# Kernel optimization log

Hardware: AMD Instinct MI355X
Metric: run time of the kernel (lower is better)

## Reference

```python
import jax, jax.numpy as jnp
import numpy as np

EPS = 1e-6  # flax.linen.LayerNorm default

def layer_norm(x, scale, bias):
    mean = jnp.mean(x, axis=-1, keepdims=True)
    var = jnp.mean(jnp.square(x - mean), axis=-1, keepdims=True)
    return (x - mean) * jax.lax.rsqrt(var + EPS) * scale + bias

def setup_inputs() -> dict:
    key = jax.random.key(0)
    ks = jax.random.split(key, 4)
    B, P, D, H = 2, 2048, 768, 12
    hd = D // H
    x = jax.random.normal(ks[0], (B, P, D), dtype=jnp.float32)
    W_qkv = jax.random.normal(ks[1], (D, 3 * D), dtype=jnp.float32) * (D ** -0.5)
    W_out = jax.random.normal(ks[2], (D, D), dtype=jnp.float32) * (D ** -0.5)
    b_out = jnp.zeros((D,), dtype=jnp.float32)
    return {
        "x": x,
        "W_qkv": W_qkv,
        "q_scale": jnp.ones((hd,), jnp.float32),
        "q_bias": jnp.zeros((hd,), jnp.float32),
        "k_scale": jnp.ones((hd,), jnp.float32),
        "k_bias": jnp.zeros((hd,), jnp.float32),
        "o_scale": jnp.ones((D,), jnp.float32),
        "o_bias": jnp.zeros((D,), jnp.float32),
        "W_out": W_out,
        "b_out": b_out,
    }

def reference(x, W_qkv, q_scale, q_bias, k_scale, k_bias, o_scale, o_bias, W_out, b_out):
    B, P, D = x.shape
    H = 12
    hd = D // H
    scale = hd ** -0.5
    # fused QKV projection, no bias
    qkv = (x @ W_qkv).reshape(B, P, 3, H, hd).transpose(2, 0, 3, 1, 4)  # [3,B,H,P,hd]
    q, k, v = qkv[0], qkv[1], qkv[2]
    # per-head QK LayerNorm over head_dim
    q = layer_norm(q, q_scale, q_bias) * scale
    k = layer_norm(k, k_scale, k_bias)
    attn = jnp.einsum("bhqd,bhkd->bhqk", q, k)
    attn = jax.nn.softmax(attn, axis=-1)
    out = jnp.einsum("bhqk,bhkd->bhqd", attn, v)  # [B,H,P,hd]
    out = jnp.swapaxes(out, 1, 2).reshape(B, P, D)
    out = layer_norm(out, o_scale, o_bias)
    return out @ W_out + b_out
```

## Files before the change

kernel.cpp:

```cpp
#include <hip/hip_runtime.h>
#include <hip/hip_bf16.h>

#define B_  2
#define P_  2048
#define D_  768
#define H_  12
#define HD_ 64
#define M_  (B_ * P_)
#define N1_ (3 * D_)

typedef __attribute__((ext_vector_type(8))) short short8;
typedef __attribute__((ext_vector_type(4))) float f32x4;
typedef __attribute__((ext_vector_type(16))) float f32x16;
typedef __attribute__((ext_vector_type(4))) unsigned u32x4;
typedef unsigned short ushort;

__device__ __forceinline__ ushort f2bf(float f) {
    unsigned u = __float_as_uint(f);
    u += 0x7fffu + ((u >> 16) & 1u);
    return (ushort)(u >> 16);
}

__device__ __forceinline__ unsigned cvtpk(float a, float b) {
    unsigned r;
    asm("v_cvt_pk_bf16_f32 %0, %1, %2" : "=v"(r) : "v"(a), "v"(b));
    return r;
}

__device__ __forceinline__ float bf2f(ushort u) {
    return __uint_as_float((unsigned)u << 16);
}

__device__ __forceinline__ int swap23(int s) {
    return (s & ~12) | ((s & 4) << 1) | ((s & 8) >> 1);
}

#define QSC_ (0.125f * 1.44269504088896340736f)

__global__ __launch_bounds__(512) void gemm_qkv_mfma(
        const float* __restrict__ x, const float* __restrict__ w,
        const float* __restrict__ qs, const float* __restrict__ qb,
        const float* __restrict__ ks, const float* __restrict__ kb,
        ushort* __restrict__ qkv) {
    __shared__ __align__(16) ushort As[128][40];
    __shared__ __align__(16) ushort Bs[128][40];

    const int tid  = threadIdx.x;
    const int lane = tid & 63;
    const int wv   = tid >> 6;
    const int quad = lane >> 4;
    const int col  = lane & 15;
    const int wr   = (wv >> 1) * 32;
    const int wc   = (wv & 1) * 64;
    const int rowBase = blockIdx.y * 128;
    const int colBase = blockIdx.x * 128;

    const int am0 = tid >> 3, ac4 = tid & 7;
    const int nB  = tid & 127, kq = tid >> 7;

    float4 apre[2];
    float  bpre[8];
    auto load_tile = [&](int kt) {
        const int k0 = kt * 32;
        apre[0] = *(const float4*)(x + (size_t)(rowBase + am0) * D_ + k0 + ac4 * 4);
        apre[1] = *(const float4*)(x + (size_t)(rowBase + am0 + 64) * D_ + k0 + ac4 * 4);
#pragma unroll
        for (int j = 0; j < 8; j++)
            bpre[j] = w[(size_t)(k0 + kq * 8 + j) * N1_ + colBase + nB];
    };

    f32x4 acc[2][4];
#pragma unroll
    for (int i = 0; i < 2; i++)
#pragma unroll
        for (int j = 0; j < 4; j++) acc[i][j] = (f32x4){0.f, 0.f, 0.f, 0.f};

    load_tile(0);
    const int NT = D_ / 32;
    for (int kt = 0; kt < NT; kt++) {
        __syncthreads();
        {
            uint2 a0 = {cvtpk(apre[0].x, apre[0].y), cvtpk(apre[0].z, apre[0].w)};
            uint2 a1 = {cvtpk(apre[1].x, apre[1].y), cvtpk(apre[1].z, apre[1].w)};
            *(uint2*)&As[am0][ac4 * 4]      = a0;
            *(uint2*)&As[am0 + 64][ac4 * 4] = a1;
            u32x4 bb;
#pragma unroll
            for (int j = 0; j < 4; j++) bb[j] = cvtpk(bpre[2 * j], bpre[2 * j + 1]);
            *(u32x4*)&Bs[nB][kq * 8] = bb;
        }
        __syncthreads();
        if (kt + 1 < NT) load_tile(kt + 1);

        short8 af[2], bf[4];
#pragma unroll
        for (int mt = 0; mt < 2; mt++) af[mt] = *(const short8*)&As[wr + mt * 16 + col][quad * 8];
#pragma unroll
        for (int nt = 0; nt < 4; nt++) bf[nt] = *(const short8*)&Bs[wc + nt * 16 + col][quad * 8];
#pragma unroll
        for (int mt = 0; mt < 2; mt++)
#pragma unroll
            for (int nt = 0; nt < 4; nt++)
                acc[mt][nt] = __builtin_amdgcn_mfma_f32_16x16x32_bf16(af[mt], bf[nt], acc[mt][nt], 0, 0, 0);
    }

    const int comp = colBase / D_;
    const int rem  = colBase + wc - comp * D_;
    const int h    = rem >> 6;
    float sc4[4] = {0, 0, 0, 0}, bi4[4] = {0, 0, 0, 0};
    if (comp == 0) {
#pragma unroll
        for (int nt = 0; nt < 4; nt++) { sc4[nt] = qs[nt * 16 + col]; bi4[nt] = qb[nt * 16 + col]; }
    } else if (comp == 1) {
#pragma unroll
        for (int nt = 0; nt < 4; nt++) { sc4[nt] = ks[nt * 16 + col]; bi4[nt] = kb[nt * 16 + col]; }
    }

#pragma unroll
    for (int mt = 0; mt < 2; mt++) {
#pragma unroll
        for (int r = 0; r < 4; r++) {
            int m  = rowBase + wr + mt * 16 + quad * 4 + r;
            int bb = m >> 11;
            int p  = m & 2047;
            float v0 = acc[mt][0][r], v1 = acc[mt][1][r], v2 = acc[mt][2][r], v3 = acc[mt][3][r];
            if (comp < 2) {
                float s = v0 + v1 + v2 + v3;
#pragma unroll
                for (int off = 1; off < 16; off <<= 1) s += __shfl_xor(s, off, 64);
                float mean = s * (1.0f / 64.0f);
                float d0 = v0 - mean, d1 = v1 - mean, d2 = v2 - mean, d3 = v3 - mean;
                float sq = d0 * d0 + d1 * d1 + d2 * d2 + d3 * d3;
#pragma unroll
                for (int off = 1; off < 16; off <<= 1) sq += __shfl_xor(sq, off, 64);
                float inv = rsqrtf(sq * (1.0f / 64.0f) + 1e-6f);
                v0 = d0 * inv * sc4[0] + bi4[0];
                v1 = d1 * inv * sc4[1] + bi4[1];
                v2 = d2 * inv * sc4[2] + bi4[2];
                v3 = d3 * inv * sc4[3] + bi4[3];
                if (comp == 0) { v0 *= QSC_; v1 *= QSC_; v2 *= QSC_; v3 *= QSC_; }
            }
            size_t base = ((((size_t)comp * B_ + bb) * H_ + h) * P_ + p) * HD_;
            qkv[base +  0 + col] = f2bf(v0);
            qkv[base + 16 + col] = f2bf(v1);
            qkv[base + 32 + col] = f2bf(v2);
            qkv[base + 48 + col] = f2bf(v3);
        }
    }
}

__global__ __launch_bounds__(256) void attn_split(const ushort* __restrict__ qkv,
                                                  ushort* __restrict__ o0, ushort* __restrict__ o1,
                                                  ushort* __restrict__ o2, ushort* __restrict__ o3,
                                                  float* __restrict__ l0, float* __restrict__ l1,
                                                  float* __restrict__ l2, float* __restrict__ l3) {
    const int p0  = blockIdx.x * 256;
    const int bh  = blockIdx.y;
    const int s   = blockIdx.z;
    const int nsp = gridDim.z;
    const int b   = bh / H_, h = bh % H_;
    ushort* opart = (s == 0) ? o0 : (s == 1) ? o1 : (s == 2) ? o2 : o3;
    float*  lpart = (s == 0) ? l0 : (s == 1) ? l1 : (s == 2) ? l2 : l3;
    const int tid  = threadIdx.x;
    const int lane = tid & 63;
    const int wv   = tid >> 6;
    const int half = lane >> 5;
    const int n32  = lane & 31;

    __shared__ __align__(16) ushort KVs[2][2][64][72];

    const size_t hs  = (size_t)P_ * HD_;
    const int    kv0 = s * (P_ / nsp);
    const ushort* qg = qkv + ((size_t)(0 * B_ + b) * H_ + h) * hs + (size_t)(p0 + wv * 64) * HD_;
    const ushort* kg = qkv + ((size_t)(1 * B_ + b) * H_ + h) * hs + (size_t)kv0 * HD_;
    const ushort* vg = qkv + ((size_t)(2 * B_ + b) * H_ + h) * hs + (size_t)kv0 * HD_;

    short8 aq[2][4];
#pragma unroll
    for (int qs2 = 0; qs2 < 2; qs2++)
#pragma unroll
        for (int ks2 = 0; ks2 < 4; ks2++)
            aq[qs2][ks2] = *(const short8*)(qg + (size_t)(qs2 * 32 + n32) * HD_ + ks2 * 16 + half * 8);

    float lsum[2] = {0.f, 0.f};
    f32x16 oaccT[2][2];
#pragma unroll
    for (int q2 = 0; q2 < 2; q2++)
#pragma unroll
        for (int nt = 0; nt < 2; nt++)
#pragma unroll
            for (int r = 0; r < 16; r++) oaccT[q2][nt][r] = 0.f;

    const int kr = tid >> 3, kc8 = tid & 7;
    const int krs = swap23(kr);
    const int vd = tid & 63,  vkh = tid >> 6;

    uint4  kpre[2];
    ushort vpre[16];
    auto load_tile = [&](int kt) {
        const ushort* kg_t = kg + (size_t)kt * 64 * HD_;
        const ushort* vg_t = vg + (size_t)kt * 64 * HD_;
        kpre[0] = *(const uint4*)(kg_t + (size_t)kr * HD_ + kc8 * 8);
        kpre[1] = *(const uint4*)(kg_t + (size_t)(kr + 32) * HD_ + kc8 * 8);
#pragma unroll
        for (int j = 0; j < 16; j++)
            vpre[j] = vg_t[(size_t)(vkh * 16 + j) * HD_ + vd];
    };
    auto stage = [&](int buf) {
        *(uint4*)&KVs[buf][0][krs][kc8 * 8]      = kpre[0];
        *(uint4*)&KVs[buf][0][krs + 32][kc8 * 8] = kpre[1];
        *(short8*)&KVs[buf][1][vd][vkh * 16]     = *(short8*)&vpre[0];
        *(short8*)&KVs[buf][1][vd][vkh * 16 + 8] = *(short8*)&vpre[8];
    };

    load_tile(0);
    stage(0);
    __syncthreads();

    const int NT = (P_ / 64) / nsp;
    int cur = 0;
    for (int kt = 0; kt < NT; kt++) {
        const bool more = (kt + 1 < NT);
        if (more) load_tile(kt + 1);

        ushort (*Ks)[72] = KVs[cur][0];
        ushort (*Vs)[72] = KVs[cur][1];

#pragma unroll
        for (int nt = 0; nt < 2; nt++) {
#pragma unroll
            for (int q2 = 0; q2 < 2; q2++) {
                f32x16 sc;
#pragma unroll
                for (int r = 0; r < 16; r++) sc[r] = 0.f;
                __builtin_amdgcn_s_setprio(1);
#pragma unroll
                for (int ks2 = 0; ks2 < 4; ks2++) {
                    short8 kb2 = *(const short8*)&Ks[nt * 32 + n32][ks2 * 16 + half * 8];
                    sc = __builtin_amdgcn_mfma_f32_32x32x16_bf16(kb2, aq[q2][ks2], sc, 0, 0, 0);
                }
                __builtin_amdgcn_s_setprio(0);
                float p[16];
#pragma unroll
                for (int r = 0; r < 16; r++) {
                    p[r] = __builtin_amdgcn_exp2f(sc[r]);
                    lsum[q2] += p[r];
                }
                unsigned w[8];
#pragma unroll
                for (int i = 0; i < 8; i++) w[i] = cvtpk(p[2 * i], p[2 * i + 1]);
                __builtin_amdgcn_s_setprio(1);
#pragma unroll
                for (int kp2 = 0; kp2 < 2; kp2++) {
                    u32x4 t = {w[kp2 * 4 + 0], w[kp2 * 4 + 1], w[kp2 * 4 + 2], w[kp2 * 4 + 3]};
                    short8 pb = __builtin_bit_cast(short8, t);
                    const int kstep = nt * 2 + kp2;
#pragma unroll
                    for (int ntd = 0; ntd < 2; ntd++) {
                        short8 av = *(const short8*)&Vs[ntd * 32 + n32][kstep * 16 + half * 8];
                        oaccT[q2][ntd] = __builtin_amdgcn_mfma_f32_32x32x16_bf16(av, pb, oaccT[q2][ntd], 0, 0, 0);
                    }
                }
                __builtin_amdgcn_s_setprio(0);
            }
        }

        if (more) {
            stage(cur ^ 1);
            __syncthreads();
            cur ^= 1;
        }
    }

#pragma unroll
    for (int q2 = 0; q2 < 2; q2++)
        lsum[q2] += __shfl_xor(lsum[q2], 32, 64);
    if (lane < 32) {
        lpart[(size_t)bh * P_ + p0 + wv * 64 +  0 + lane] = lsum[0];
        lpart[(size_t)bh * P_ + p0 + wv * 64 + 32 + lane] = lsum[1];
    }

    float* scr = (float*)&KVs[0][0][0][0] + wv * 1152;
#pragma unroll
    for (int q2 = 0; q2 < 2; q2++) {
#pragma unroll
        for (int ntd = 0; ntd < 2; ntd++) {
#pragma unroll
            for (int r = 0; r < 16; r++)
                scr[n32 * 36 + (r & 3) + 8 * (r >> 2) + 4 * half] = oaccT[q2][ntd][r];
#pragma unroll
            for (int i = 0; i < 4; i++) {
                int ql = i * 8 + (lane >> 3);
                int c4 = lane & 7;
                float4 v = *(const float4*)&scr[ql * 36 + c4 * 4];
                uint2 pk = {cvtpk(v.x, v.y), cvtpk(v.z, v.w)};
                *(uint2*)(opart + ((size_t)bh * P_ + p0 + wv * 64 + q2 * 32 + ql) * HD_ + ntd * 32 + c4 * 4) = pk;
            }
        }
    }
}

__global__ __launch_bounds__(256) void ln_o(const ushort* __restrict__ o0,
                                            const ushort* __restrict__ o1,
                                            const ushort* __restrict__ o2,
                                            const ushort* __restrict__ o3,
                                            const float* __restrict__ l0,
                                            const float* __restrict__ l1,
                                            const float* __restrict__ l2,
                                            const float* __restrict__ l3,
                                            const int ns,
                                            ushort* __restrict__ lnb,
                                            const float* __restrict__ osc,
                                            const float* __restrict__ ob) {
    __shared__ float red[4];
    __shared__ float red2[4];
    const int row = blockIdx.x;
    const int b   = row >> 11;
    const int p   = row & (P_ - 1);
    const int tid = threadIdx.x;

    auto src = [&](int d) {
        int h = d >> 6;
        size_t lr  = (size_t)(b * H_ + h) * P_ + p;
        size_t idx = lr * HD_ + (d & 63);
        float num = bf2f(o0[idx]) + bf2f(o1[idx]);
        float den = l0[lr] + l1[lr];
        if (ns == 4) { num += bf2f(o2[idx]) + bf2f(o3[idx]); den += l2[lr] + l3[lr]; }
        return num / den;
    };
    float v0 = src(tid);
    float v1 = src(tid + 256);
    float v2 = src(tid + 512);
    float s = v0 + v1 + v2;
#pragma unroll
    for (int o = 32; o > 0; o >>= 1) s += __shfl_xor(s, o, 64);
    if ((tid & 63) == 0) red[tid >> 6] = s;
    __syncthreads();
    float mean = (red[0] + red[1] + red[2] + red[3]) * (1.0f / 768.0f);
    float d0 = v0 - mean, d1 = v1 - mean, d2 = v2 - mean;
    float sq = d0 * d0 + d1 * d1 + d2 * d2;
#pragma unroll
    for (int o = 32; o > 0; o >>= 1) sq += __shfl_xor(sq, o, 64);
    if ((tid & 63) == 0) red2[tid >> 6] = sq;
    __syncthreads();
    float var = (red2[0] + red2[1] + red2[2] + red2[3]) * (1.0f / 768.0f);
    float inv = rsqrtf(var + 1e-6f);
    const size_t base = (size_t)row * D_;
    lnb[base + tid]       = f2bf(d0 * inv * osc[tid]       + ob[tid]);
    lnb[base + tid + 256] = f2bf(d1 * inv * osc[tid + 256] + ob[tid + 256]);
    lnb[base + tid + 512] = f2bf(d2 * inv * osc[tid + 512] + ob[tid + 512]);
}

__global__ __launch_bounds__(256) void gemm_out_mfma(
        const ushort* __restrict__ a, const float* __restrict__ w,
        const float* __restrict__ bias, float* __restrict__ out) {
    __shared__ __align__(16) ushort As[64][40];
    __shared__ __align__(16) ushort Bs[64][40];

    const int tid  = threadIdx.x;
    const int lane = tid & 63;
    const int wv   = tid >> 6;
    const int quad = lane >> 4;
    const int col  = lane & 15;
    const int wr   = (wv >> 1) * 32;
    const int wc   = (wv & 1) * 32;
    const int rowBase = blockIdx.y * 64;
    const int colBase = blockIdx.x * 64;

    const int am  = tid >> 2, ac8 = tid & 3;
    const int nB  = tid & 63, kq = tid >> 6;

    uint4 apre;
    float bpre[8];
    auto load_tile = [&](int kt) {
        const int k0 = kt * 32;
        apre = *(const uint4*)(a + (size_t)(rowBase + am) * D_ + k0 + ac8 * 8);
#pragma unroll
        for (int j = 0; j < 8; j++)
            bpre[j] = w[(size_t)(k0 + kq * 8 + j) * D_ + colBase + nB];
    };

    f32x4 acc[2][2];
#pragma unroll
    for (int i = 0; i < 2; i++)
#pragma unroll
        for (int j = 0; j < 2; j++) acc[i][j] = (f32x4){0.f, 0.f, 0.f, 0.f};

    load_tile(0);
    const int NT = D_ / 32;
    for (int kt = 0; kt < NT; kt++) {
        __syncthreads();
        *(uint4*)&As[am][ac8 * 8] = apre;
        {
            u32x4 bb;
#pragma unroll
            for (int j = 0; j < 4; j++) bb[j] = cvtpk(bpre[2 * j], bpre[2 * j + 1]);
            *(u32x4*)&Bs[nB][kq * 8] = bb;
        }
        __syncthreads();
        if (kt + 1 < NT) load_tile(kt + 1);

        short8 af[2], bf[2];
#pragma unroll
        for (int mt = 0; mt < 2; mt++) af[mt] = *(const short8*)&As[wr + mt * 16 + col][quad * 8];
#pragma unroll
        for (int nt = 0; nt < 2; nt++) bf[nt] = *(const short8*)&Bs[wc + nt * 16 + col][quad * 8];
#pragma unroll
        for (int mt = 0; mt < 2; mt++)
#pragma unroll
            for (int nt = 0; nt < 2; nt++)
                acc[mt][nt] = __builtin_amdgcn_mfma_f32_16x16x32_bf16(af[mt], bf[nt], acc[mt][nt], 0, 0, 0);
    }

    float b2[2];
#pragma unroll
    for (int nt = 0; nt < 2; nt++) b2[nt] = bias[colBase + wc + nt * 16 + col];
#pragma unroll
    for (int mt = 0; mt < 2; mt++) {
#pragma unroll
        for (int r = 0; r < 4; r++) {
            int m = rowBase + wr + mt * 16 + quad * 4 + r;
            float* dst = out + (size_t)m * D_ + colBase + wc;
#pragma unroll
            for (int nt = 0; nt < 2; nt++)
                dst[nt * 16 + col] = acc[mt][nt][r] + b2[nt];
        }
    }
}

extern "C" void kernel_launch(void* const* d_in, const int* in_sizes, int n_in,
                              void* d_out, int out_size, void* d_ws, size_t ws_size,
                              hipStream_t stream) {
    const float* x    = (const float*)d_in[0];
    const float* Wqkv = (const float*)d_in[1];
    const float* qs   = (const float*)d_in[2];
    const float* qb   = (const float*)d_in[3];
    const float* ks   = (const float*)d_in[4];
    const float* kb   = (const float*)d_in[5];
    const float* osc  = (const float*)d_in[6];
    const float* ob   = (const float*)d_in[7];
    const float* Wout = (const float*)d_in[8];
    const float* bout = (const float*)d_in[9];
    float* out = (float*)d_out;

    ushort* qkv = (ushort*)d_ws;
    const size_t qkvE = (size_t)3 * B_ * H_ * P_ * HD_;
    const size_t oE   = (size_t)B_ * H_ * P_ * HD_;
    const size_t lE   = (size_t)B_ * H_ * P_;
    ushort* obase = qkv + qkvE;
    const size_t need4 = (qkvE + 3 * oE) * sizeof(ushort) + 4 * lE * sizeof(float);
    const int nsp = (ws_size >= need4) ? 4 : 2;
    ushort* op[4];
    float* lbase;
    if (nsp == 4) {
        op[0] = obase; op[1] = obase + oE; op[2] = obase + 2 * oE; op[3] = (ushort*)out;
        lbase = (float*)(obase + 3 * oE);
    } else {
        op[0] = obase; op[1] = (ushort*)out; op[2] = obase; op[3] = obase;
        lbase = (float*)(obase + oE);
    }
    float* lp[4] = {lbase, lbase + lE, lbase + 2 * lE, lbase + 3 * lE};
    ushort* ln_buf = qkv;

    gemm_qkv_mfma<<<dim3(N1_ / 128, M_ / 128), 512, 0, stream>>>(x, Wqkv, qs, qb, ks, kb, qkv);
    attn_split<<<dim3(P_ / 256, B_ * H_, nsp), 256, 0, stream>>>(
        qkv, op[0], op[1], op[2], op[3], lp[0], lp[1], lp[2], lp[3]);
    ln_o<<<dim3(M_), 256, 0, stream>>>(
        op[0], op[1], op[2], op[3], lp[0], lp[1], lp[2], lp[3], nsp, ln_buf, osc, ob);
    gemm_out_mfma<<<dim3(D_ / 64, M_ / 64), 256, 0, stream>>>(ln_buf, Wout, bout, out);
}
```

Measured before the change: 197.4 us.

## Split attention work across eight waves of 32 queries each

The attention kernel now launches 512 threads per block, so each of eight waves owns 32 query rows instead of four waves owning 64. This halves per-thread accumulators, Q fragments and K/V prefetch registers, and each thread stages half as much of every K/V tile. The aim is more resident waves to hide LDS and global-memory latency. The cost is that each K/V fragment read from LDS now feeds half as many MFMAs, so LDS traffic per MFMA doubles. A barrier is added before the shared tile buffer is reused as output scratch.

```diff
diff --git a/kernel.cpp b/kernel.cpp
--- a/kernel.cpp
+++ b/kernel.cpp
@@ -149,7 +149,7 @@
     }
 }
 
-__global__ __launch_bounds__(256) void attn_split(const ushort* __restrict__ qkv,
+__global__ __launch_bounds__(512) void attn_split(const ushort* __restrict__ qkv,
                                                   ushort* __restrict__ o0, ushort* __restrict__ o1,
                                                   ushort* __restrict__ o2, ushort* __restrict__ o3,
                                                   float* __restrict__ l0, float* __restrict__ l1,
@@ -171,46 +171,39 @@
 
     const size_t hs  = (size_t)P_ * HD_;
     const int    kv0 = s * (P_ / nsp);
-    const ushort* qg = qkv + ((size_t)(0 * B_ + b) * H_ + h) * hs + (size_t)(p0 + wv * 64) * HD_;
+    const ushort* qg = qkv + ((size_t)(0 * B_ + b) * H_ + h) * hs + (size_t)(p0 + wv * 32) * HD_;
     const ushort* kg = qkv + ((size_t)(1 * B_ + b) * H_ + h) * hs + (size_t)kv0 * HD_;
     const ushort* vg = qkv + ((size_t)(2 * B_ + b) * H_ + h) * hs + (size_t)kv0 * HD_;
 
-    short8 aq[2][4];
-#pragma unroll
-    for (int qs2 = 0; qs2 < 2; qs2++)
-#pragma unroll
-        for (int ks2 = 0; ks2 < 4; ks2++)
-            aq[qs2][ks2] = *(const short8*)(qg + (size_t)(qs2 * 32 + n32) * HD_ + ks2 * 16 + half * 8);
-
-    float lsum[2] = {0.f, 0.f};
-    f32x16 oaccT[2][2];
-#pragma unroll
-    for (int q2 = 0; q2 < 2; q2++)
-#pragma unroll
-        for (int nt = 0; nt < 2; nt++)
-#pragma unroll
-            for (int r = 0; r < 16; r++) oaccT[q2][nt][r] = 0.f;
+    short8 aq[4];
+#pragma unroll
+    for (int ks2 = 0; ks2 < 4; ks2++)
+        aq[ks2] = *(const short8*)(qg + (size_t)n32 * HD_ + ks2 * 16 + half * 8);
+
+    float lsum = 0.f;
+    f32x16 oaccT[2];
+#pragma unroll
+    for (int nt = 0; nt < 2; nt++)
+#pragma unroll
+        for (int r = 0; r < 16; r++) oaccT[nt][r] = 0.f;
 
     const int kr = tid >> 3, kc8 = tid & 7;
     const int krs = swap23(kr);
     const int vd = tid & 63,  vkh = tid >> 6;
 
-    uint4  kpre[2];
-    ushort vpre[16];
+    uint4  kpre;
+    ushort vpre[8];
     auto load_tile = [&](int kt) {
         const ushort* kg_t = kg + (size_t)kt * 64 * HD_;
         const ushort* vg_t = vg + (size_t)kt * 64 * HD_;
-        kpre[0] = *(const uint4*)(kg_t + (size_t)kr * HD_ + kc8 * 8);
-        kpre[1] = *(const uint4*)(kg_t + (size_t)(kr + 32) * HD_ + kc8 * 8);
-#pragma unroll
-        for (int j = 0; j < 16; j++)
-            vpre[j] = vg_t[(size_t)(vkh * 16 + j) * HD_ + vd];
+        kpre = *(const uint4*)(kg_t + (size_t)kr * HD_ + kc8 * 8);
+#pragma unroll
+        for (int j = 0; j < 8; j++)
+            vpre[j] = vg_t[(size_t)(vkh * 8 + j) * HD_ + vd];
     };
     auto stage = [&](int buf) {
-        *(uint4*)&KVs[buf][0][krs][kc8 * 8]      = kpre[0];
-        *(uint4*)&KVs[buf][0][krs + 32][kc8 * 8] = kpre[1];
-        *(short8*)&KVs[buf][1][vd][vkh * 16]     = *(short8*)&vpre[0];
-        *(short8*)&KVs[buf][1][vd][vkh * 16 + 8] = *(short8*)&vpre[8];
+        *(uint4*)&KVs[buf][0][krs][kc8 * 8] = kpre;
+        *(short8*)&KVs[buf][1][vd][vkh * 8] = *(short8*)&vpre[0];
     };
 
     load_tile(0);
@@ -228,41 +221,38 @@
 
 #pragma unroll
         for (int nt = 0; nt < 2; nt++) {
-#pragma unroll
-            for (int q2 = 0; q2 < 2; q2++) {
-                f32x16 sc;
-#pragma unroll
-                for (int r = 0; r < 16; r++) sc[r] = 0.f;
-                __builtin_amdgcn_s_setprio(1);
-#pragma unroll
-                for (int ks2 = 0; ks2 < 4; ks2++) {
-                    short8 kb2 = *(const short8*)&Ks[nt * 32 + n32][ks2 * 16 + half * 8];
-                    sc = __builtin_amdgcn_mfma_f32_32x32x16_bf16(kb2, aq[q2][ks2], sc, 0, 0, 0);
+            f32x16 sc;
+#pragma unroll
+            for (int r = 0; r < 16; r++) sc[r] = 0.f;
+            __builtin_amdgcn_s_setprio(1);
+#pragma unroll
+            for (int ks2 = 0; ks2 < 4; ks2++) {
+                short8 kb2 = *(const short8*)&Ks[nt * 32 + n32][ks2 * 16 + half * 8];
+                sc = __builtin_amdgcn_mfma_f32_32x32x16_bf16(kb2, aq[ks2], sc, 0, 0, 0);
+            }
+            __builtin_amdgcn_s_setprio(0);
+            float p[16];
+#pragma unroll
+            for (int r = 0; r < 16; r++) {
+                p[r] = __builtin_amdgcn_exp2f(sc[r]);
+                lsum += p[r];
+            }
+            unsigned w[8];
+#pragma unroll
+            for (int i = 0; i < 8; i++) w[i] = cvtpk(p[2 * i], p[2 * i + 1]);
+            __builtin_amdgcn_s_setprio(1);
+#pragma unroll
+            for (int kp2 = 0; kp2 < 2; kp2++) {
+                u32x4 t = {w[kp2 * 4 + 0], w[kp2 * 4 + 1], w[kp2 * 4 + 2], w[kp2 * 4 + 3]};
+                short8 pb = __builtin_bit_cast(short8, t);
+                const int kstep = nt * 2 + kp2;
+#pragma unroll
+                for (int ntd = 0; ntd < 2; ntd++) {
+                    short8 av = *(const short8*)&Vs[ntd * 32 + n32][kstep * 16 + half * 8];
+                    oaccT[ntd] = __builtin_amdgcn_mfma_f32_32x32x16_bf16(av, pb, oaccT[ntd], 0, 0, 0);
                 }
-                __builtin_amdgcn_s_setprio(0);
-                float p[16];
-#pragma unroll
-                for (int r = 0; r < 16; r++) {
-                    p[r] = __builtin_amdgcn_exp2f(sc[r]);
-                    lsum[q2] += p[r];
-                }
-                unsigned w[8];
-#pragma unroll
-                for (int i = 0; i < 8; i++) w[i] = cvtpk(p[2 * i], p[2 * i + 1]);
-                __builtin_amdgcn_s_setprio(1);
-#pragma unroll
-                for (int kp2 = 0; kp2 < 2; kp2++) {
-                    u32x4 t = {w[kp2 * 4 + 0], w[kp2 * 4 + 1], w[kp2 * 4 + 2], w[kp2 * 4 + 3]};
-                    short8 pb = __builtin_bit_cast(short8, t);
-                    const int kstep = nt * 2 + kp2;
-#pragma unroll
-                    for (int ntd = 0; ntd < 2; ntd++) {
-                        short8 av = *(const short8*)&Vs[ntd * 32 + n32][kstep * 16 + half * 8];
-                        oaccT[q2][ntd] = __builtin_amdgcn_mfma_f32_32x32x16_bf16(av, pb, oaccT[q2][ntd], 0, 0, 0);
-                    }
-                }
-                __builtin_amdgcn_s_setprio(0);
             }
+            __builtin_amdgcn_s_setprio(0);
         }
 
         if (more) {
@@ -272,30 +262,24 @@
         }
     }
 
-#pragma unroll
-    for (int q2 = 0; q2 < 2; q2++)
-        lsum[q2] += __shfl_xor(lsum[q2], 32, 64);
-    if (lane < 32) {
-        lpart[(size_t)bh * P_ + p0 + wv * 64 +  0 + lane] = lsum[0];
-        lpart[(size_t)bh * P_ + p0 + wv * 64 + 32 + lane] = lsum[1];
-    }
-
+    lsum += __shfl_xor(lsum, 32, 64);
+    if (lane < 32)
+        lpart[(size_t)bh * P_ + p0 + wv * 32 + lane] = lsum;
+
+    __syncthreads();
     float* scr = (float*)&KVs[0][0][0][0] + wv * 1152;
 #pragma unroll
-    for (int q2 = 0; q2 < 2; q2++) {
-#pragma unroll
-        for (int ntd = 0; ntd < 2; ntd++) {
-#pragma unroll
-            for (int r = 0; r < 16; r++)
-                scr[n32 * 36 + (r & 3) + 8 * (r >> 2) + 4 * half] = oaccT[q2][ntd][r];
-#pragma unroll
-            for (int i = 0; i < 4; i++) {
-                int ql = i * 8 + (lane >> 3);
-                int c4 = lane & 7;
-                float4 v = *(const float4*)&scr[ql * 36 + c4 * 4];
-                uint2 pk = {cvtpk(v.x, v.y), cvtpk(v.z, v.w)};
-                *(uint2*)(opart + ((size_t)bh * P_ + p0 + wv * 64 + q2 * 32 + ql) * HD_ + ntd * 32 + c4 * 4) = pk;
-            }
+    for (int ntd = 0; ntd < 2; ntd++) {
+#pragma unroll
+        for (int r = 0; r < 16; r++)
+            scr[n32 * 36 + (r & 3) + 8 * (r >> 2) + 4 * half] = oaccT[ntd][r];
+#pragma unroll
+        for (int i = 0; i < 4; i++) {
+            int ql = i * 8 + (lane >> 3);
+            int c4 = lane & 7;
+            float4 v = *(const float4*)&scr[ql * 36 + c4 * 4];
+            uint2 pk = {cvtpk(v.x, v.y), cvtpk(v.z, v.w)};
+            *(uint2*)(opart + ((size_t)bh * P_ + p0 + wv * 32 + ql) * HD_ + ntd * 32 + c4 * 4) = pk;
         }
     }
 }
@@ -463,7 +447,7 @@
     ushort* ln_buf = qkv;
 
     gemm_qkv_mfma<<<dim3(N1_ / 128, M_ / 128), 512, 0, stream>>>(x, Wqkv, qs, qb, ks, kb, qkv);
-    attn_split<<<dim3(P_ / 256, B_ * H_, nsp), 256, 0, stream>>>(
+    attn_split<<<dim3(P_ / 256, B_ * H_, nsp), 512, 0, stream>>>(
         qkv, op[0], op[1], op[2], op[3], lp[0], lp[1], lp[2], lp[3]);
     ln_o<<<dim3(M_), 256, 0, stream>>>(
         op[0], op[1], op[2], op[3], lp[0], lp[1], lp[2], lp[3], nsp, ln_buf, osc, ob);
```

Result: faster. 184.0 us (-6.8%).
